# Kernel optimization log

Hardware: AMD Instinct MI355X
Metric: run time of the kernel (lower is better)

The kernel has to match this reference:

```python
import jax, jax.numpy as jnp
import numpy as np

NUM_GROUPS = 4
EPS = 1e-6


def group_norm(x, gamma, beta):
    # x: [B, C, H, W, L]
    b, ch = x.shape[0], x.shape[1]
    xr = x.reshape(b, NUM_GROUPS, ch // NUM_GROUPS, -1)
    mean = xr.mean(axis=(2, 3), keepdims=True)
    var = xr.var(axis=(2, 3), keepdims=True)
    xn = ((xr - mean) * jax.lax.rsqrt(var + EPS)).reshape(x.shape)
    return xn * gamma.reshape(1, ch, 1, 1, 1) + beta.reshape(1, ch, 1, 1, 1)


def conv1(x, w, bias):
    # 1x1x1 Conv3d == channel-mixing linear: w [Cout, Cin]
    return jnp.einsum('bchwl,oc->bohwl', x, w) + bias.reshape(1, -1, 1, 1, 1)


def setup_inputs() -> dict:
    key = jax.random.key(0)
    ks = jax.random.split(key, 16)
    C = 128
    shp = (2, C, 16, 16, 16)
    scale = 1.0 / np.sqrt(C)
    inp = {
        'x': jax.random.normal(ks[0], shp, dtype=jnp.float32),
        'c': jax.random.normal(ks[1], shp, dtype=jnp.float32),
        'g1': jnp.ones((C,), jnp.float32),
        'b1': jnp.zeros((C,), jnp.float32),
        'g2': jnp.ones((C,), jnp.float32),
        'b2': jnp.zeros((C,), jnp.float32),
        'wq': jax.random.normal(ks[2], (C, C), jnp.float32) * scale,
        'bq': jnp.zeros((C,), jnp.float32),
        'wk': jax.random.normal(ks[3], (C, C), jnp.float32) * scale,
        'bk': jnp.zeros((C,), jnp.float32),
        'wv': jax.random.normal(ks[4], (C, C), jnp.float32) * scale,
        'bv': jnp.zeros((C,), jnp.float32),
        'wp': jax.random.normal(ks[5], (C, C), jnp.float32) * scale,
        'bp': jnp.zeros((C,), jnp.float32),
    }
    return inp


def reference(x, c, g1, b1, g2, b2, wq, bq, wk, bk, wv, bv, wp, bp):
    h_ = group_norm(x, g1, b1)   # norm_1(x)
    c_ = group_norm(c, g2, b2)   # norm_2(c)
    q = conv1(c_, wq, bq)        # query from conditioning c
    k = conv1(h_, wk, bk)
    v = conv1(h_, wv, bv)
    b, ch, h, w, l = q.shape
    n = h * w * l
    qf = q.reshape(b, ch, n)
    kf = k.reshape(b, ch, n)
    vf = v.reshape(b, ch, n)
    # scores[b, i, j] = <q[:, i], k[:, j]> * C^-0.5
    scores = jnp.einsum('bci,bcj->bij', qf, kf) * (ch ** -0.5)
    attn = jax.nn.softmax(scores, axis=2)
    # out[b, c, i] = sum_j v[b, c, j] * attn[b, i, j]
    out = jnp.einsum('bcj,bij->bci', vf, attn).reshape(b, ch, h, w, l)
    out = conv1(out, wp, bp)
    return x + out
```

## Files before the change

### kernel.cpp

```cpp
#include <hip/hip_runtime.h>
#include <math.h>

#define C 128
#define N 4096
#define B 2
#define CPG 32

typedef __attribute__((ext_vector_type(8))) short bf16x8;
typedef __attribute__((ext_vector_type(4))) float f32x4;

static __device__ __forceinline__ ushort f2bf(float f) {
  unsigned u = __float_as_uint(f);
  unsigned r = (u + 0x7fffu + ((u >> 16) & 1u)) >> 16;
  return (ushort)r;
}

__global__ __launch_bounds__(256) void gn_partial_kernel(
    const float* __restrict__ x, const float* __restrict__ cc,
    const float* __restrict__ wq, const float* __restrict__ wk,
    const float* __restrict__ wv, const float* __restrict__ wp,
    float* __restrict__ stats, ushort* __restrict__ wb) {
  if (blockIdx.y == 2) {
    if (blockIdx.x >= 32) return;
    int idx = (blockIdx.x * 256 + threadIdx.x) * 8;
    const float* srcs[4] = {wq, wk, wv, wp};
    const float* s = srcs[idx >> 14] + (idx & 16383);
    float4 a = *(const float4*)s;
    float4 b2 = *(const float4*)(s + 4);
    ushort h[8];
    h[0] = f2bf(a.x);  h[1] = f2bf(a.y);  h[2] = f2bf(a.z);  h[3] = f2bf(a.w);
    h[4] = f2bf(b2.x); h[5] = f2bf(b2.y); h[6] = f2bf(b2.z); h[7] = f2bf(b2.w);
    *(uint4*)(wb + idx) = *(uint4*)h;
    return;
  }
  const int t = blockIdx.y;
  const int bg = blockIdx.x >> 3, slice = blockIdx.x & 7;
  const float* in = (t == 0) ? x : cc;
  const float4* base = (const float4*)(in + (size_t)bg * CPG * N + slice * 16384);
  float s = 0.f, sq = 0.f;
  #pragma unroll
  for (int k = 0; k < 16; ++k) {
    float4 v = base[threadIdx.x + k * 256];
    s  += v.x + v.y + v.z + v.w;
    sq += v.x * v.x + v.y * v.y + v.z * v.z + v.w * v.w;
  }
  #pragma unroll
  for (int off = 32; off > 0; off >>= 1) {
    s  += __shfl_down(s, off, 64);
    sq += __shfl_down(sq, off, 64);
  }
  __shared__ float ss[4], ssq[4];
  const int wid = threadIdx.x >> 6;
  if ((threadIdx.x & 63) == 0) { ss[wid] = s; ssq[wid] = sq; }
  __syncthreads();
  if (threadIdx.x == 0) {
    atomicAdd(&stats[(t * 8 + bg) * 2 + 0], ss[0] + ss[1] + ss[2] + ss[3]);
    atomicAdd(&stats[(t * 8 + bg) * 2 + 1], ssq[0] + ssq[1] + ssq[2] + ssq[3]);
  }
}

__global__ __launch_bounds__(256) void qkv_kernel(
    const float* __restrict__ x, const float* __restrict__ cc,
    const float* __restrict__ g1, const float* __restrict__ b1,
    const float* __restrict__ g2, const float* __restrict__ b2,
    const ushort* __restrict__ wqb, const ushort* __restrict__ wkb,
    const ushort* __restrict__ wvb,
    const float* __restrict__ bq, const float* __restrict__ bk,
    const float* __restrict__ bv, const float* __restrict__ stats,
    ushort* __restrict__ qt, ushort* __restrict__ kt, ushort* __restrict__ vb) {
  const int zw    = blockIdx.y;
  const int which = zw >> 1;
  const int b     = zw & 1;
  const int i0    = blockIdx.x * 32;
  const int tid   = threadIdx.x;

  const float *in, *bias, *gamma, *beta;
  const ushort* wmat;
  int tensor;
  if (which == 0)      { in = cc; wmat = wqb; bias = bq; gamma = g2; beta = b2; tensor = 1; }
  else if (which == 1) { in = x;  wmat = wkb; bias = bk; gamma = g1; beta = b1; tensor = 0; }
  else                 { in = x;  wmat = wvb; bias = bv; gamma = g1; beta = b1; tensor = 0; }

  __shared__ float a_s[C], d_s[C];
  __shared__ __align__(16) ushort xt[32 * 136];
  if (tid < C) {
    const int ch = tid, g = ch >> 5;
    const float cnt = (float)(CPG * N);
    float S  = stats[(tensor * 8 + b * 4 + g) * 2 + 0];
    float SQ = stats[(tensor * 8 + b * 4 + g) * 2 + 1];
    float mean = S / cnt;
    float var  = SQ / cnt - mean * mean;
    float rstd = rsqrtf(var + 1e-6f);
    float ga = gamma[ch];
    a_s[ch] = rstd * ga;
    d_s[ch] = beta[ch] - mean * rstd * ga;
  }
  __syncthreads();

  {
    const int c = tid >> 1, ih = tid & 1;
    const float* src = in + ((size_t)b * C + c) * N + i0 + ih * 16;
    const float av = a_s[c], dv = d_s[c];
    #pragma unroll
    for (int k4 = 0; k4 < 4; ++k4) {
      float4 v = *(const float4*)(src + k4 * 4);
      const int i = ih * 16 + k4 * 4;
      xt[(i + 0) * 136 + c] = f2bf(fmaf(v.x, av, dv));
      xt[(i + 1) * 136 + c] = f2bf(fmaf(v.y, av, dv));
      xt[(i + 2) * 136 + c] = f2bf(fmaf(v.z, av, dv));
      xt[(i + 3) * 136 + c] = f2bf(fmaf(v.w, av, dv));
    }
  }
  __syncthreads();

  const int w = tid >> 6, lane = tid & 63, quad = lane >> 4, l15 = lane & 15;
  bf16x8 aw[2][4];
  #pragma unroll
  for (int mt2 = 0; mt2 < 2; ++mt2)
    #pragma unroll
    for (int ks = 0; ks < 4; ++ks)
      aw[mt2][ks] = *(const bf16x8*)(wmat + (size_t)(w * 32 + mt2 * 16 + l15) * 128 + ks * 32 + quad * 8);

  f32x4 acc[2][2];
  #pragma unroll
  for (int mt2 = 0; mt2 < 2; ++mt2)
    #pragma unroll
    for (int nt = 0; nt < 2; ++nt) acc[mt2][nt] = (f32x4){0.f, 0.f, 0.f, 0.f};

  #pragma unroll
  for (int nt = 0; nt < 2; ++nt) {
    bf16x8 bo[4];
    #pragma unroll
    for (int ks = 0; ks < 4; ++ks)
      bo[ks] = *(const bf16x8*)(&xt[(nt * 16 + l15) * 136 + ks * 32 + quad * 8]);
    #pragma unroll
    for (int mt2 = 0; mt2 < 2; ++mt2)
      #pragma unroll
      for (int ks = 0; ks < 4; ++ks)
        acc[mt2][nt] = __builtin_amdgcn_mfma_f32_16x16x32_bf16(aw[mt2][ks], bo[ks], acc[mt2][nt], 0, 0, 0);
  }

  #pragma unroll
  for (int mt2 = 0; mt2 < 2; ++mt2) {
    const int ob = w * 32 + mt2 * 16 + quad * 4;
    float4 bb4 = *(const float4*)(bias + ob);
    float bbv[4] = {bb4.x, bb4.y, bb4.z, bb4.w};
    #pragma unroll
    for (int nt = 0; nt < 2; ++nt) {
      const int i = i0 + nt * 16 + l15;
      if (which <= 1) {
        ushort* dst = (which == 0 ? qt : kt);
        ushort h[4];
        #pragma unroll
        for (int r = 0; r < 4; ++r) h[r] = f2bf(acc[mt2][nt][r] + bbv[r]);
        *(uint2*)(dst + ((size_t)b * N + i) * C + ob) = *(uint2*)h;
      } else {
        #pragma unroll
        for (int r = 0; r < 4; ++r)
          vb[((size_t)b * C + ob + r) * N + i] = f2bf(acc[mt2][nt][r] + bbv[r]);
      }
    }
  }
}

__global__ __launch_bounds__(256) void attn_kernel(
    const ushort* __restrict__ qt, const ushort* __restrict__ kt,
    const ushort* __restrict__ vb, float* __restrict__ pml,
    ushort* __restrict__ pO, int part_keys) {
  __shared__ __align__(16) ushort ksts[32 * 136];
  __shared__ __align__(16) ushort vss [128 * 40];
  __shared__ __align__(16) ushort pss [4][16 * 40];

  const int b    = blockIdx.z;
  const int part = blockIdx.y;
  const int i0   = blockIdx.x * 64;
  const int tid  = threadIdx.x;
  const int w    = tid >> 6;
  const int lane = tid & 63;
  const int quad = lane >> 4;
  const int l15  = lane & 15;
  const float scale = 0.08838834764831845f;

  bf16x8 aq[4];
  {
    const ushort* qrow = qt + ((size_t)b * N + i0 + w * 16 + l15) * C;
    #pragma unroll
    for (int ks = 0; ks < 4; ++ks)
      aq[ks] = *(const bf16x8*)(qrow + ks * 32 + quad * 8);
  }

  float lacc[4] = {0.f, 0.f, 0.f, 0.f};
  f32x4 Ofr[8];
  #pragma unroll
  for (int mt = 0; mt < 8; ++mt) Ofr[mt] = (f32x4){0.f, 0.f, 0.f, 0.f};

  const int krow = tid >> 3, kseg = tid & 7;
  const int vc = tid >> 1, vseg = tid & 1;
  const ushort* kbase = kt + ((size_t)b * N + krow) * C + kseg * 16;
  const ushort* vbase = vb + ((size_t)b * C + vc) * N + vseg * 16;
  uint4* dk = (uint4*)(&ksts[krow * 136 + kseg * 16]);
  uint4* dv = (uint4*)(&vss[vc * 40 + vseg * 16]);

  const int tcount = part_keys >> 5;
  const int jbase = part * part_keys;
  uint4 k0, k1, v0, v1;
  {
    const uint4* sk = (const uint4*)(kbase + (size_t)jbase * C);
    k0 = sk[0]; k1 = sk[1];
    const uint4* sv = (const uint4*)(vbase + jbase);
    v0 = sv[0]; v1 = sv[1];
  }

  for (int t = 0; t < tcount; ++t) {
    __syncthreads();
    dk[0] = k0; dk[1] = k1;
    dv[0] = v0; dv[1] = v1;
    __syncthreads();
    if (t + 1 < tcount) {
      const int j1 = jbase + (t + 1) * 32;
      const uint4* sk = (const uint4*)(kbase + (size_t)j1 * C);
      k0 = sk[0]; k1 = sk[1];
      const uint4* sv = (const uint4*)(vbase + j1);
      v0 = sv[0]; v1 = sv[1];
    }

    f32x4 sfr[2];
    #pragma unroll
    for (int nt = 0; nt < 2; ++nt) {
      f32x4 s = (f32x4){0.f, 0.f, 0.f, 0.f};
      #pragma unroll
      for (int ks = 0; ks < 4; ++ks) {
        bf16x8 bk = *(const bf16x8*)(&ksts[(nt * 16 + l15) * 136 + ks * 32 + quad * 8]);
        s = __builtin_amdgcn_mfma_f32_16x16x32_bf16(aq[ks], bk, s, 0, 0, 0);
      }
      sfr[nt] = s;
    }

    #pragma unroll
    for (int r = 0; r < 4; ++r) {
      float p0 = __expf(sfr[0][r] * scale);
      float p1 = __expf(sfr[1][r] * scale);
      pss[w][(quad * 4 + r) * 40 + l15]      = f2bf(p0);
      pss[w][(quad * 4 + r) * 40 + 16 + l15] = f2bf(p1);
      lacc[r] += p0 + p1;
    }
    bf16x8 bpf = *(const bf16x8*)(&pss[w][l15 * 40 + quad * 8]);
    #pragma unroll
    for (int mt = 0; mt < 8; ++mt) {
      bf16x8 av = *(const bf16x8*)(&vss[(mt * 16 + l15) * 40 + quad * 8]);
      Ofr[mt] = __builtin_amdgcn_mfma_f32_16x16x32_bf16(av, bpf, Ofr[mt], 0, 0, 0);
    }
  }

  #pragma unroll
  for (int off = 1; off < 16; off <<= 1)
    #pragma unroll
    for (int r = 0; r < 4; ++r)
      lacc[r] += __shfl_xor(lacc[r], off, 64);

  const size_t blk = ((size_t)part * 64 + blockIdx.x) * 2 + b;
  if (l15 == 0) {
    float* lb = pml + blk * 64;
    #pragma unroll
    for (int r = 0; r < 4; ++r)
      lb[w * 16 + quad * 4 + r] = lacc[r];
  }
  ushort* ob = pO + blk * 8192;
  const int irow = w * 16 + l15;
  #pragma unroll
  for (int mt = 0; mt < 8; ++mt) {
    ushort h[4];
    #pragma unroll
    for (int r = 0; r < 4; ++r) h[r] = f2bf(Ofr[mt][r]);
    *(uint2*)(ob + irow * 128 + mt * 16 + quad * 4) = *(uint2*)h;
  }
}

__global__ __launch_bounds__(256) void combine_kernel(
    const float* __restrict__ x, const float* __restrict__ bp,
    const ushort* __restrict__ wpb, const float* __restrict__ pml,
    const ushort* __restrict__ pO, float* __restrict__ out, int nparts) {
  __shared__ __align__(16) ushort obf[32 * 136];
  __shared__ float linv_s[32];
  const int qt32 = blockIdx.x, b = blockIdx.y;
  const int qt64 = qt32 >> 1, rowoff = (qt32 & 1) * 32;
  const int tid = threadIdx.x;

  if (tid < 32) {
    const int row = rowoff + tid;
    float sum = 0.f;
    for (int p = 0; p < nparts; ++p) {
      const size_t blk = ((size_t)p * 64 + qt64) * 2 + b;
      sum += pml[blk * 64 + row];
    }
    linv_s[tid] = 1.f / sum;
  }
  __syncthreads();

  const int lrow = tid >> 3, seg = tid & 7;
  const int prow = rowoff + lrow;
  float acc[16];
  #pragma unroll
  for (int j = 0; j < 16; ++j) acc[j] = 0.f;
  for (int p = 0; p < nparts; ++p) {
    const size_t blk = ((size_t)p * 64 + qt64) * 2 + b;
    const ushort* src = pO + blk * 8192 + prow * 128 + seg * 16;
    uint4 u[2];
    u[0] = *(const uint4*)src;
    u[1] = *(const uint4*)(src + 8);
    const ushort* hs = (const ushort*)u;
    #pragma unroll
    for (int j = 0; j < 16; ++j)
      acc[j] += __uint_as_float(((unsigned)hs[j]) << 16);
  }
  {
    const float linv = linv_s[lrow];
    ushort h[16];
    #pragma unroll
    for (int j = 0; j < 16; ++j) h[j] = f2bf(acc[j] * linv);
    uint4* d = (uint4*)(&obf[lrow * 136 + seg * 16]);
    d[0] = ((uint4*)h)[0];
    d[1] = ((uint4*)h)[1];
  }
  __syncthreads();

  const int w = tid >> 6, lane = tid & 63, quad = lane >> 4, l15 = lane & 15;
  const int i0 = qt32 * 32;
  bf16x8 awp[2][4];
  #pragma unroll
  for (int mt2 = 0; mt2 < 2; ++mt2)
    #pragma unroll
    for (int ks = 0; ks < 4; ++ks)
      awp[mt2][ks] = *(const bf16x8*)(wpb + (size_t)(w * 32 + mt2 * 16 + l15) * 128 + ks * 32 + quad * 8);

  #pragma unroll
  for (int nt = 0; nt < 2; ++nt) {
    bf16x8 bo[4];
    #pragma unroll
    for (int ks = 0; ks < 4; ++ks)
      bo[ks] = *(const bf16x8*)(&obf[(nt * 16 + l15) * 136 + ks * 32 + quad * 8]);
    #pragma unroll
    for (int mt2 = 0; mt2 < 2; ++mt2) {
      f32x4 acc2 = (f32x4){0.f, 0.f, 0.f, 0.f};
      #pragma unroll
      for (int ks = 0; ks < 4; ++ks)
        acc2 = __builtin_amdgcn_mfma_f32_16x16x32_bf16(awp[mt2][ks], bo[ks], acc2, 0, 0, 0);
      #pragma unroll
      for (int r = 0; r < 4; ++r) {
        const int o = w * 32 + mt2 * 16 + quad * 4 + r;
        const int i = i0 + nt * 16 + l15;
        const size_t off = ((size_t)b * C + o) * (size_t)N + i;
        out[off] = x[off] + acc2[r] + bp[o];
      }
    }
  }
}

extern "C" void kernel_launch(void* const* d_in, const int* in_sizes, int n_in,
                              void* d_out, int out_size, void* d_ws, size_t ws_size,
                              hipStream_t stream) {
  const float* x  = (const float*)d_in[0];
  const float* cc = (const float*)d_in[1];
  const float* g1 = (const float*)d_in[2];
  const float* b1 = (const float*)d_in[3];
  const float* g2 = (const float*)d_in[4];
  const float* b2 = (const float*)d_in[5];
  const float* wq = (const float*)d_in[6];
  const float* bq = (const float*)d_in[7];
  const float* wk = (const float*)d_in[8];
  const float* bk = (const float*)d_in[9];
  const float* wv = (const float*)d_in[10];
  const float* bv = (const float*)d_in[11];
  const float* wp = (const float*)d_in[12];
  const float* bp = (const float*)d_in[13];
  float* out = (float*)d_out;

  const size_t BNC = (size_t)B * N * C;
  char* base = (char*)d_ws;
  float* stats = (float*)base;
  ushort* qt = (ushort*)(base + 4096);
  ushort* kt = qt + BNC;
  ushort* vb = kt + BNC;
  ushort* wb = vb + BNC;
  ushort* wqb = wb, *wkb = wb + 16384, *wvb = wb + 32768, *wpb = wb + 49152;
  float* pml = (float*)(wb + 65536);

  const size_t fixed = 4096 + 3 * BNC * 2 + 131072;
  const size_t per_part = (size_t)64 * 2 * (8192 * 2 + 256);
  const int nparts = (ws_size >= fixed + 8 * per_part) ? 8
                   : (ws_size >= fixed + 4 * per_part) ? 4 : 2;
  ushort* pO = (ushort*)((char*)pml + (size_t)nparts * 32768);
  const int part_keys = N / nparts;

  hipMemsetAsync(stats, 0, 128, stream);
  gn_partial_kernel<<<dim3(64, 3), 256, 0, stream>>>(x, cc, wq, wk, wv, wp, stats, wb);
  qkv_kernel<<<dim3(128, 6), 256, 0, stream>>>(x, cc, g1, b1, g2, b2,
                                               wqb, wkb, wvb, bq, bk, bv, stats,
                                               qt, kt, vb);
  attn_kernel<<<dim3(64, nparts, 2), 256, 0, stream>>>(qt, kt, vb, pml, pO, part_keys);
  combine_kernel<<<dim3(128, 2), 256, 0, stream>>>(x, bp, wpb, pml, pO, out, nparts);
}
```

Measured before the change: 141.2 us.

## Double-buffer attention K/V tiles, widen query tile, fuse K/V projection, drop atomics

Each attention block now handles 128 query rows, two 16-row tiles per wave, so every K/V tile staged in shared memory feeds twice as many MFMAs. K/V staging is double-buffered, which cuts the two barriers per step to one. The QKV kernel computes K and V from a single normalized x tile instead of normalizing x twice. GroupNorm partial sums are written per slice instead of added atomically, which removes the memset. The costs are more registers and shared memory per block, half as many attention blocks, and a launch-bounds hint of 3 blocks per SM that may cause spills.

```diff
diff --git a/kernel.cpp b/kernel.cpp
--- a/kernel.cpp
+++ b/kernel.cpp
@@ -54,8 +54,8 @@
   if ((threadIdx.x & 63) == 0) { ss[wid] = s; ssq[wid] = sq; }
   __syncthreads();
   if (threadIdx.x == 0) {
-    atomicAdd(&stats[(t * 8 + bg) * 2 + 0], ss[0] + ss[1] + ss[2] + ss[3]);
-    atomicAdd(&stats[(t * 8 + bg) * 2 + 1], ssq[0] + ssq[1] + ssq[2] + ssq[3]);
+    stats[((t * 8 + bg) * 8 + slice) * 2 + 0] = ss[0] + ss[1] + ss[2] + ss[3];
+    stats[((t * 8 + bg) * 8 + slice) * 2 + 1] = ssq[0] + ssq[1] + ssq[2] + ssq[3];
   }
 }
 
@@ -68,26 +68,28 @@
     const float* __restrict__ bq, const float* __restrict__ bk,
     const float* __restrict__ bv, const float* __restrict__ stats,
     ushort* __restrict__ qt, ushort* __restrict__ kt, ushort* __restrict__ vb) {
-  const int zw    = blockIdx.y;
-  const int which = zw >> 1;
-  const int b     = zw & 1;
+  const int z     = blockIdx.z;
+  const int b     = blockIdx.y;
   const int i0    = blockIdx.x * 32;
   const int tid   = threadIdx.x;
-
-  const float *in, *bias, *gamma, *beta;
-  const ushort* wmat;
-  int tensor;
-  if (which == 0)      { in = cc; wmat = wqb; bias = bq; gamma = g2; beta = b2; tensor = 1; }
-  else if (which == 1) { in = x;  wmat = wkb; bias = bk; gamma = g1; beta = b1; tensor = 0; }
-  else                 { in = x;  wmat = wvb; bias = bv; gamma = g1; beta = b1; tensor = 0; }
+  const int nm    = z ? 2 : 1;
+
+  const float* in    = z ? x : cc;
+  const float* gamma = z ? g1 : g2;
+  const float* beta  = z ? b1 : b2;
+  const int tensor   = z ? 0 : 1;
 
   __shared__ float a_s[C], d_s[C];
   __shared__ __align__(16) ushort xt[32 * 136];
   if (tid < C) {
     const int ch = tid, g = ch >> 5;
     const float cnt = (float)(CPG * N);
-    float S  = stats[(tensor * 8 + b * 4 + g) * 2 + 0];
-    float SQ = stats[(tensor * 8 + b * 4 + g) * 2 + 1];
+    float S = 0.f, SQ = 0.f;
+    #pragma unroll
+    for (int sl = 0; sl < 8; ++sl) {
+      S  += stats[((tensor * 8 + b * 4 + g) * 8 + sl) * 2 + 0];
+      SQ += stats[((tensor * 8 + b * 4 + g) * 8 + sl) * 2 + 1];
+    }
     float mean = S / cnt;
     float var  = SQ / cnt - mean * mean;
     float rstd = rsqrtf(var + 1e-6f);
@@ -114,18 +116,24 @@
   __syncthreads();
 
   const int w = tid >> 6, lane = tid & 63, quad = lane >> 4, l15 = lane & 15;
-  bf16x8 aw[2][4];
-  #pragma unroll
-  for (int mt2 = 0; mt2 < 2; ++mt2)
-    #pragma unroll
-    for (int ks = 0; ks < 4; ++ks)
-      aw[mt2][ks] = *(const bf16x8*)(wmat + (size_t)(w * 32 + mt2 * 16 + l15) * 128 + ks * 32 + quad * 8);
-
-  f32x4 acc[2][2];
-  #pragma unroll
-  for (int mt2 = 0; mt2 < 2; ++mt2)
-    #pragma unroll
-    for (int nt = 0; nt < 2; ++nt) acc[mt2][nt] = (f32x4){0.f, 0.f, 0.f, 0.f};
+  const ushort* wmats[2];
+  wmats[0] = z ? wkb : wqb;
+  wmats[1] = wvb;
+
+  bf16x8 aw[2][2][4];
+  for (int m = 0; m < nm; ++m)
+    #pragma unroll
+    for (int mt2 = 0; mt2 < 2; ++mt2)
+      #pragma unroll
+      for (int ks = 0; ks < 4; ++ks)
+        aw[m][mt2][ks] = *(const bf16x8*)(wmats[m] + (size_t)(w * 32 + mt2 * 16 + l15) * 128 + ks * 32 + quad * 8);
+
+  f32x4 acc[2][2][2];
+  for (int m = 0; m < nm; ++m)
+    #pragma unroll
+    for (int mt2 = 0; mt2 < 2; ++mt2)
+      #pragma unroll
+      for (int nt = 0; nt < 2; ++nt) acc[m][mt2][nt] = (f32x4){0.f, 0.f, 0.f, 0.f};
 
   #pragma unroll
   for (int nt = 0; nt < 2; ++nt) {
@@ -133,47 +141,51 @@
     #pragma unroll
     for (int ks = 0; ks < 4; ++ks)
       bo[ks] = *(const bf16x8*)(&xt[(nt * 16 + l15) * 136 + ks * 32 + quad * 8]);
-    #pragma unroll
-    for (int mt2 = 0; mt2 < 2; ++mt2)
-      #pragma unroll
-      for (int ks = 0; ks < 4; ++ks)
-        acc[mt2][nt] = __builtin_amdgcn_mfma_f32_16x16x32_bf16(aw[mt2][ks], bo[ks], acc[mt2][nt], 0, 0, 0);
-  }
-
-  #pragma unroll
-  for (int mt2 = 0; mt2 < 2; ++mt2) {
-    const int ob = w * 32 + mt2 * 16 + quad * 4;
-    float4 bb4 = *(const float4*)(bias + ob);
-    float bbv[4] = {bb4.x, bb4.y, bb4.z, bb4.w};
-    #pragma unroll
-    for (int nt = 0; nt < 2; ++nt) {
-      const int i = i0 + nt * 16 + l15;
-      if (which <= 1) {
-        ushort* dst = (which == 0 ? qt : kt);
-        ushort h[4];
+    for (int m = 0; m < nm; ++m)
+      #pragma unroll
+      for (int mt2 = 0; mt2 < 2; ++mt2)
         #pragma unroll
-        for (int r = 0; r < 4; ++r) h[r] = f2bf(acc[mt2][nt][r] + bbv[r]);
-        *(uint2*)(dst + ((size_t)b * N + i) * C + ob) = *(uint2*)h;
-      } else {
-        #pragma unroll
-        for (int r = 0; r < 4; ++r)
-          vb[((size_t)b * C + ob + r) * N + i] = f2bf(acc[mt2][nt][r] + bbv[r]);
+        for (int ks = 0; ks < 4; ++ks)
+          acc[m][mt2][nt] = __builtin_amdgcn_mfma_f32_16x16x32_bf16(aw[m][mt2][ks], bo[ks], acc[m][mt2][nt], 0, 0, 0);
+  }
+
+  for (int m = 0; m < nm; ++m) {
+    const float* bias = z ? (m == 0 ? bk : bv) : bq;
+    #pragma unroll
+    for (int mt2 = 0; mt2 < 2; ++mt2) {
+      const int ob = w * 32 + mt2 * 16 + quad * 4;
+      float4 bb4 = *(const float4*)(bias + ob);
+      float bbv[4] = {bb4.x, bb4.y, bb4.z, bb4.w};
+      #pragma unroll
+      for (int nt = 0; nt < 2; ++nt) {
+        const int i = i0 + nt * 16 + l15;
+        if (m == 0) {
+          ushort* dst = z ? kt : qt;
+          ushort h[4];
+          #pragma unroll
+          for (int r = 0; r < 4; ++r) h[r] = f2bf(acc[m][mt2][nt][r] + bbv[r]);
+          *(uint2*)(dst + ((size_t)b * N + i) * C + ob) = *(uint2*)h;
+        } else {
+          #pragma unroll
+          for (int r = 0; r < 4; ++r)
+            vb[((size_t)b * C + ob + r) * N + i] = f2bf(acc[m][mt2][nt][r] + bbv[r]);
+        }
       }
     }
   }
 }
 
-__global__ __launch_bounds__(256) void attn_kernel(
+__global__ __launch_bounds__(256, 3) void attn_kernel(
     const ushort* __restrict__ qt, const ushort* __restrict__ kt,
     const ushort* __restrict__ vb, float* __restrict__ pml,
     ushort* __restrict__ pO, int part_keys) {
-  __shared__ __align__(16) ushort ksts[32 * 136];
-  __shared__ __align__(16) ushort vss [128 * 40];
-  __shared__ __align__(16) ushort pss [4][16 * 40];
+  __shared__ __align__(16) ushort ksts[2][32 * 136];
+  __shared__ __align__(16) ushort vss [2][128 * 40];
+  __shared__ __align__(16) ushort pss [4][2][16 * 40];
 
   const int b    = blockIdx.z;
   const int part = blockIdx.y;
-  const int i0   = blockIdx.x * 64;
+  const int i0   = blockIdx.x * 128;
   const int tid  = threadIdx.x;
   const int w    = tid >> 6;
   const int lane = tid & 63;
@@ -181,41 +193,44 @@
   const int l15  = lane & 15;
   const float scale = 0.08838834764831845f;
 
-  bf16x8 aq[4];
-  {
-    const ushort* qrow = qt + ((size_t)b * N + i0 + w * 16 + l15) * C;
+  bf16x8 aq[2][4];
+  #pragma unroll
+  for (int rt = 0; rt < 2; ++rt) {
+    const ushort* qrow = qt + ((size_t)b * N + i0 + w * 32 + rt * 16 + l15) * C;
     #pragma unroll
     for (int ks = 0; ks < 4; ++ks)
-      aq[ks] = *(const bf16x8*)(qrow + ks * 32 + quad * 8);
-  }
-
-  float lacc[4] = {0.f, 0.f, 0.f, 0.f};
-  f32x4 Ofr[8];
-  #pragma unroll
-  for (int mt = 0; mt < 8; ++mt) Ofr[mt] = (f32x4){0.f, 0.f, 0.f, 0.f};
+      aq[rt][ks] = *(const bf16x8*)(qrow + ks * 32 + quad * 8);
+  }
+
+  float lacc[2][4] = {{0.f, 0.f, 0.f, 0.f}, {0.f, 0.f, 0.f, 0.f}};
+  f32x4 Ofr[2][8];
+  #pragma unroll
+  for (int rt = 0; rt < 2; ++rt)
+    #pragma unroll
+    for (int mt = 0; mt < 8; ++mt) Ofr[rt][mt] = (f32x4){0.f, 0.f, 0.f, 0.f};
 
   const int krow = tid >> 3, kseg = tid & 7;
   const int vc = tid >> 1, vseg = tid & 1;
   const ushort* kbase = kt + ((size_t)b * N + krow) * C + kseg * 16;
   const ushort* vbase = vb + ((size_t)b * C + vc) * N + vseg * 16;
-  uint4* dk = (uint4*)(&ksts[krow * 136 + kseg * 16]);
-  uint4* dv = (uint4*)(&vss[vc * 40 + vseg * 16]);
 
   const int tcount = part_keys >> 5;
   const int jbase = part * part_keys;
+
   uint4 k0, k1, v0, v1;
   {
     const uint4* sk = (const uint4*)(kbase + (size_t)jbase * C);
     k0 = sk[0]; k1 = sk[1];
     const uint4* sv = (const uint4*)(vbase + jbase);
     v0 = sv[0]; v1 = sv[1];
-  }
+    uint4* dk = (uint4*)(&ksts[0][krow * 136 + kseg * 16]);
+    dk[0] = k0; dk[1] = k1;
+    uint4* dv = (uint4*)(&vss[0][vc * 40 + vseg * 16]);
+    dv[0] = v0; dv[1] = v1;
+  }
+  int cur = 0;
 
   for (int t = 0; t < tcount; ++t) {
-    __syncthreads();
-    dk[0] = k0; dk[1] = k1;
-    dv[0] = v0; dv[1] = v1;
-    __syncthreads();
     if (t + 1 < tcount) {
       const int j1 = jbase + (t + 1) * 32;
       const uint4* sk = (const uint4*)(kbase + (size_t)j1 * C);
@@ -223,56 +238,79 @@
       const uint4* sv = (const uint4*)(vbase + j1);
       v0 = sv[0]; v1 = sv[1];
     }
-
-    f32x4 sfr[2];
+    __syncthreads();
+
+    f32x4 sfr[2][2];
     #pragma unroll
     for (int nt = 0; nt < 2; ++nt) {
-      f32x4 s = (f32x4){0.f, 0.f, 0.f, 0.f};
+      f32x4 s0 = (f32x4){0.f, 0.f, 0.f, 0.f};
+      f32x4 s1 = (f32x4){0.f, 0.f, 0.f, 0.f};
       #pragma unroll
       for (int ks = 0; ks < 4; ++ks) {
-        bf16x8 bk = *(const bf16x8*)(&ksts[(nt * 16 + l15) * 136 + ks * 32 + quad * 8]);
-        s = __builtin_amdgcn_mfma_f32_16x16x32_bf16(aq[ks], bk, s, 0, 0, 0);
+        bf16x8 bkf = *(const bf16x8*)(&ksts[cur][(nt * 16 + l15) * 136 + ks * 32 + quad * 8]);
+        s0 = __builtin_amdgcn_mfma_f32_16x16x32_bf16(aq[0][ks], bkf, s0, 0, 0, 0);
+        s1 = __builtin_amdgcn_mfma_f32_16x16x32_bf16(aq[1][ks], bkf, s1, 0, 0, 0);
       }
-      sfr[nt] = s;
-    }
-
-    #pragma unroll
-    for (int r = 0; r < 4; ++r) {
-      float p0 = __expf(sfr[0][r] * scale);
-      float p1 = __expf(sfr[1][r] * scale);
-      pss[w][(quad * 4 + r) * 40 + l15]      = f2bf(p0);
-      pss[w][(quad * 4 + r) * 40 + 16 + l15] = f2bf(p1);
-      lacc[r] += p0 + p1;
-    }
-    bf16x8 bpf = *(const bf16x8*)(&pss[w][l15 * 40 + quad * 8]);
+      sfr[0][nt] = s0; sfr[1][nt] = s1;
+    }
+
+    #pragma unroll
+    for (int rt = 0; rt < 2; ++rt)
+      #pragma unroll
+      for (int r = 0; r < 4; ++r) {
+        float p0 = __expf(sfr[rt][0][r] * scale);
+        float p1 = __expf(sfr[rt][1][r] * scale);
+        pss[w][rt][(quad * 4 + r) * 40 + l15]      = f2bf(p0);
+        pss[w][rt][(quad * 4 + r) * 40 + 16 + l15] = f2bf(p1);
+        lacc[rt][r] += p0 + p1;
+      }
+
+    bf16x8 bpf0 = *(const bf16x8*)(&pss[w][0][l15 * 40 + quad * 8]);
+    bf16x8 bpf1 = *(const bf16x8*)(&pss[w][1][l15 * 40 + quad * 8]);
     #pragma unroll
     for (int mt = 0; mt < 8; ++mt) {
-      bf16x8 av = *(const bf16x8*)(&vss[(mt * 16 + l15) * 40 + quad * 8]);
-      Ofr[mt] = __builtin_amdgcn_mfma_f32_16x16x32_bf16(av, bpf, Ofr[mt], 0, 0, 0);
+      bf16x8 av = *(const bf16x8*)(&vss[cur][(mt * 16 + l15) * 40 + quad * 8]);
+      Ofr[0][mt] = __builtin_amdgcn_mfma_f32_16x16x32_bf16(av, bpf0, Ofr[0][mt], 0, 0, 0);
+      Ofr[1][mt] = __builtin_amdgcn_mfma_f32_16x16x32_bf16(av, bpf1, Ofr[1][mt], 0, 0, 0);
+    }
+
+    if (t + 1 < tcount) {
+      cur ^= 1;
+      uint4* dk = (uint4*)(&ksts[cur][krow * 136 + kseg * 16]);
+      dk[0] = k0; dk[1] = k1;
+      uint4* dv = (uint4*)(&vss[cur][vc * 40 + vseg * 16]);
+      dv[0] = v0; dv[1] = v1;
     }
   }
 
   #pragma unroll
   for (int off = 1; off < 16; off <<= 1)
     #pragma unroll
-    for (int r = 0; r < 4; ++r)
-      lacc[r] += __shfl_xor(lacc[r], off, 64);
-
-  const size_t blk = ((size_t)part * 64 + blockIdx.x) * 2 + b;
+    for (int rt = 0; rt < 2; ++rt)
+      #pragma unroll
+      for (int r = 0; r < 4; ++r)
+        lacc[rt][r] += __shfl_xor(lacc[rt][r], off, 64);
+
+  const size_t blk = ((size_t)part * 32 + blockIdx.x) * 2 + b;
   if (l15 == 0) {
-    float* lb = pml + blk * 64;
-    #pragma unroll
-    for (int r = 0; r < 4; ++r)
-      lb[w * 16 + quad * 4 + r] = lacc[r];
-  }
-  ushort* ob = pO + blk * 8192;
-  const int irow = w * 16 + l15;
-  #pragma unroll
-  for (int mt = 0; mt < 8; ++mt) {
-    ushort h[4];
-    #pragma unroll
-    for (int r = 0; r < 4; ++r) h[r] = f2bf(Ofr[mt][r]);
-    *(uint2*)(ob + irow * 128 + mt * 16 + quad * 4) = *(uint2*)h;
+    float* lb = pml + blk * 128;
+    #pragma unroll
+    for (int rt = 0; rt < 2; ++rt)
+      #pragma unroll
+      for (int r = 0; r < 4; ++r)
+        lb[w * 32 + rt * 16 + quad * 4 + r] = lacc[rt][r];
+  }
+  ushort* ob = pO + blk * 16384;
+  #pragma unroll
+  for (int rt = 0; rt < 2; ++rt) {
+    const int irow = w * 32 + rt * 16 + l15;
+    #pragma unroll
+    for (int mt = 0; mt < 8; ++mt) {
+      ushort h[4];
+      #pragma unroll
+      for (int r = 0; r < 4; ++r) h[r] = f2bf(Ofr[rt][mt][r]);
+      *(uint2*)(ob + irow * 128 + mt * 16 + quad * 4) = *(uint2*)h;
+    }
   }
 }
 
@@ -283,15 +321,15 @@
   __shared__ __align__(16) ushort obf[32 * 136];
   __shared__ float linv_s[32];
   const int qt32 = blockIdx.x, b = blockIdx.y;
-  const int qt64 = qt32 >> 1, rowoff = (qt32 & 1) * 32;
+  const int qt128 = qt32 >> 2, rowoff = (qt32 & 3) * 32;
   const int tid = threadIdx.x;
 
   if (tid < 32) {
     const int row = rowoff + tid;
     float sum = 0.f;
     for (int p = 0; p < nparts; ++p) {
-      const size_t blk = ((size_t)p * 64 + qt64) * 2 + b;
-      sum += pml[blk * 64 + row];
+      const size_t blk = ((size_t)p * 32 + qt128) * 2 + b;
+      sum += pml[blk * 128 + row];
     }
     linv_s[tid] = 1.f / sum;
   }
@@ -303,8 +341,8 @@
   #pragma unroll
   for (int j = 0; j < 16; ++j) acc[j] = 0.f;
   for (int p = 0; p < nparts; ++p) {
-    const size_t blk = ((size_t)p * 64 + qt64) * 2 + b;
-    const ushort* src = pO + blk * 8192 + prow * 128 + seg * 16;
+    const size_t blk = ((size_t)p * 32 + qt128) * 2 + b;
+    const ushort* src = pO + blk * 16384 + prow * 128 + seg * 16;
     uint4 u[2];
     u[0] = *(const uint4*)src;
     u[1] = *(const uint4*)(src + 8);
@@ -386,17 +424,16 @@
   float* pml = (float*)(wb + 65536);
 
   const size_t fixed = 4096 + 3 * BNC * 2 + 131072;
-  const size_t per_part = (size_t)64 * 2 * (8192 * 2 + 256);
+  const size_t per_part = 32768 + (size_t)32 * 2 * 16384 * 2;
   const int nparts = (ws_size >= fixed + 8 * per_part) ? 8
                    : (ws_size >= fixed + 4 * per_part) ? 4 : 2;
   ushort* pO = (ushort*)((char*)pml + (size_t)nparts * 32768);
   const int part_keys = N / nparts;
 
-  hipMemsetAsync(stats, 0, 128, stream);
   gn_partial_kernel<<<dim3(64, 3), 256, 0, stream>>>(x, cc, wq, wk, wv, wp, stats, wb);
-  qkv_kernel<<<dim3(128, 6), 256, 0, stream>>>(x, cc, g1, b1, g2, b2,
-                                               wqb, wkb, wvb, bq, bk, bv, stats,
-                                               qt, kt, vb);
-  attn_kernel<<<dim3(64, nparts, 2), 256, 0, stream>>>(qt, kt, vb, pml, pO, part_keys);
+  qkv_kernel<<<dim3(128, 2, 2), 256, 0, stream>>>(x, cc, g1, b1, g2, b2,
+                                                  wqb, wkb, wvb, bq, bk, bv, stats,
+                                                  qt, kt, vb);
+  attn_kernel<<<dim3(32, nparts, 2), 256, 0, stream>>>(qt, kt, vb, pml, pO, part_keys);
   combine_kernel<<<dim3(128, 2), 256, 0, stream>>>(x, bp, wpb, pml, pO, out, nparts);
 }
```

Result: slower. 147.3 us (+4.3%).
